# Optimization experiments

Hardware: AMD Instinct MI355X
Metric: run time of the kernel (lower is better)

The kernel has to match this reference:

```python
import jax, jax.numpy as jnp
import numpy as np

B, L, N = 16, 512, 32          # batch, seq_length, feature_size
E = 128                        # embed_size == frequency_size (number_frequency=1)
EMB = 8                        # embedding_dim
FCH = 64                       # fc_hidden_dim
H = 256                        # hidden_size
PRE = 96                       # pre_length
LAMBDA = 0.01                  # sparsity_threshold
SCALE = 0.02                   # init_scale


def softshrink(v, lambd=LAMBDA):
    return jnp.where(v > lambd, v - lambd, jnp.where(v < -lambd, v + lambd, 0.0))


def setup_inputs() -> dict:
    key = jax.random.key(0)
    ks = jax.random.split(key, 16)
    f32 = jnp.float32
    return {
        "x": jax.random.normal(ks[0], (B, L, N), f32),
        "emb": jax.random.normal(ks[1], (1, E), f32),
        "w0": SCALE * jax.random.normal(ks[2], (2, E, E), f32),
        "b0": SCALE * jax.random.normal(ks[3], (2, E), f32),
        "w1": SCALE * jax.random.normal(ks[4], (2, E, E), f32),
        "b1": SCALE * jax.random.normal(ks[5], (2, E), f32),
        "w2": SCALE * jax.random.normal(ks[6], (2, E, E), f32),
        "b2": SCALE * jax.random.normal(ks[7], (2, E), f32),
        "emb10": jax.random.normal(ks[8], (L, EMB), f32),
        "fc1_w": jax.random.normal(ks[9], (FCH, E * EMB), f32) / np.sqrt(E * EMB),
        "fc1_b": jnp.zeros((FCH,), f32),
        "fc2_w": jax.random.normal(ks[10], (H, FCH), f32) / np.sqrt(FCH),
        "fc2_b": jnp.zeros((H,), f32),
        "fc3_w": jax.random.normal(ks[11], (PRE, H), f32) / np.sqrt(H),
        "fc3_b": jnp.zeros((PRE,), f32),
    }


def _diag(w):
    # einsum 'bli,ii->bli' multiplies by the DIAGONAL of w only
    return jnp.diagonal(w, axis1=-2, axis2=-1)


def reference(x, emb, w0, b0, w1, b1, w2, b2, emb10,
              fc1_w, fc1_b, fc2_w, fc2_b, fc3_w, fc3_b):
    Bb = x.shape[0]
    xt = jnp.transpose(x, (0, 2, 1)).reshape(Bb, -1)          # [B, N*L]
    tok = xt[:, :, None] * emb                                 # [B, N*L, E]
    xf = jnp.fft.rfft(tok, axis=1, norm="ortho")               # [B, N*L//2+1, E] complex
    bias = xf

    # --- fourierGC (faithful to the torch op ordering, incl. o_real reuse) ---
    relu = jax.nn.relu
    d00, d01 = _diag(w0[0]), _diag(w0[1])
    o_r = relu(xf.real * d00 - xf.imag * d01 + b0[0])
    o_i = relu(xf.imag * d00 + xf.real * d01 + b0[1])
    prev = softshrink(jnp.stack([o_r, o_i], axis=-1))

    # middle layer (num_layers=3 -> one): note o_i uses the UPDATED o_r, as in torch
    d10, d11 = _diag(w1[0]), _diag(w1[1])
    o_r_new = relu(o_r * d10 - o_i * d11 + b1[0])
    o_i = relu(o_i * d10 + o_r_new * d11 + b1[1])
    o_r = o_r_new
    prev = softshrink(jnp.stack([o_r, o_i], axis=-1)) + prev

    # last layer
    d20, d21 = _diag(w2[0]), _diag(w2[1])
    o_r_new = relu(o_r * d20 - o_i * d21 + b2[0])
    o_i = relu(o_i * d20 + o_r_new * d21 + b2[1])
    z = softshrink(jnp.stack([o_r_new, o_i], axis=-1)) + prev
    zc = jax.lax.complex(z[..., 0], z[..., 1])

    xf = zc + bias
    xt = jnp.fft.irfft(xf, n=N * L, axis=1, norm="ortho")      # [B, N*L, E]
    xt = xt.reshape(Bb, N, L, E)
    xt = jnp.transpose(xt, (0, 1, 3, 2))                        # [B, N, E, L]
    h = jnp.matmul(xt, emb10)                                   # [B, N, E, EMB]
    h = h.reshape(Bb, N, E * EMB)

    lrelu = lambda v: jax.nn.leaky_relu(v, 0.01)
    h = lrelu(h @ fc1_w.T + fc1_b)
    h = lrelu(h @ fc2_w.T + fc2_b)
    out = h @ fc3_w.T + fc3_b                                   # [B, N, PRE]
    return out[:, 0, :]                                         # target_idx = 0
```

## Files before the change

### kernel.cpp

```cpp
#include <hip/hip_runtime.h>
#include <math.h>

#define Bsz   16
#define Lseq  512
#define Nfeat 32
#define E     128
#define EMB   8
#define FCH   64
#define Hd    256
#define PRE   96
#define M     16384
#define MH    8193
#define LAMBDA 0.01f

#define OFF_G   0
#define OFF_CS  524288
#define OFF_P   655376

#define TWO_PI_M   3.83495196971410293e-4f
#define TWO_PI_128 4.90873852123405245e-2f

__global__ __launch_bounds__(256)
void k_prep(const float* __restrict__ x, const float* __restrict__ emb10,
            float* __restrict__ ws) {
  __shared__ float smem[Lseq * EMB];
  int bid = blockIdx.x, tid = threadIdx.x;
  if (bid < 1025) {
    for (int i = tid; i < Lseq * EMB; i += 256) smem[i] = emb10[i];
    __syncthreads();
    int floc = tid >> 5, tl = tid & 31;
    int f = bid * 8 + floc;
    if (f > 8192) return;
    float ca[EMB], sa[EMB];
    #pragma unroll
    for (int m = 0; m < EMB; ++m) { ca[m] = 0.f; sa[m] = 0.f; }
    #pragma unroll 4
    for (int i = 0; i < 16; ++i) {
      int t = tl + 32 * i;
      int k = (f * t) & (M - 1);
      float ss, cc;
      sincosf((float)k * TWO_PI_M, &ss, &cc);
      const float* er = smem + t * EMB;
      #pragma unroll
      for (int m = 0; m < EMB; ++m) {
        ca[m] = fmaf(cc, er[m], ca[m]);
        sa[m] = fmaf(ss, er[m], sa[m]);
      }
    }
    #pragma unroll
    for (int off = 16; off >= 1; off >>= 1) {
      #pragma unroll
      for (int m = 0; m < EMB; ++m) {
        ca[m] += __shfl_xor(ca[m], off, 64);
        sa[m] += __shfl_xor(sa[m], off, 64);
      }
    }
    if (tl == 0) {
      float wf = (f == 0 || f == 8192) ? (1.0f / 128.0f) : (2.0f / 128.0f);
      float* o = ws + OFF_CS + f * 16;
      #pragma unroll
      for (int m = 0; m < EMB; ++m) { o[m] = ca[m] * wf; o[8 + m] = sa[m] * wf; }
    }
  } else {
    int v = bid - 1025;
    int b = v >> 6, t1base = (v & 63) << 1;
    int t1loc = tid >> 7, idx = tid & 127;
    {
      int t = (t1base + t1loc) + 128 * idx;
      int n = t >> 9, l = t & 511;
      smem[t1loc * 128 + idx] = x[b * (Lseq * Nfeat) + l * Nfeat + n];
    }
    __syncthreads();
    int f1 = idx, t1 = t1base + t1loc;
    float s1, c1; sincosf((float)f1 * TWO_PI_128, &s1, &c1);
    float c2 = c1 * c1 - s1 * s1, s2 = 2.f * s1 * c1;
    float cA = 1.f, sA = 0.f, cB = c1, sB = s1;
    float grA = 0.f, giA = 0.f, grB = 0.f, giB = 0.f;
    const float* xc = smem + t1loc * 128;
    #pragma unroll 8
    for (int t2 = 0; t2 < 128; t2 += 2) {
      float x0 = xc[t2], x1 = xc[t2 + 1];
      grA = fmaf(x0, cA, grA); giA = fmaf(x0, -sA, giA);
      grB = fmaf(x1, cB, grB); giB = fmaf(x1, -sB, giB);
      float cn = cA * c2 - sA * s2; sA = sA * c2 + cA * s2; cA = cn;
      cn = cB * c2 - sB * s2;       sB = sB * c2 + cB * s2; cB = cn;
    }
    float gr = grA + grB, gi = giA + giB;
    float sb, cb; sincosf((float)(f1 * t1) * TWO_PI_M, &sb, &cb);
    float grr = gr * cb + gi * sb;
    float gii = gi * cb - gr * sb;
    float* G = ws + OFF_G + ((b * 128 + f1) * 128 + t1) * 2;
    G[0] = grr;
    G[1] = gii;
  }
}

__global__ __launch_bounds__(256)
void k_gcf(const float* __restrict__ emb,
           const float* __restrict__ w0, const float* __restrict__ b0,
           const float* __restrict__ w1, const float* __restrict__ b1,
           const float* __restrict__ w2, const float* __restrict__ b2,
           float* __restrict__ ws) {
  int f1 = blockIdx.x, b = blockIdx.y, tid = threadIdx.x;
  int nf2 = (f1 == 0) ? 65 : 64;
  __shared__ float2 Gs[128];
  __shared__ float Xp[4][65][2];
  __shared__ float CSs[65 * 16];
  {
    const float2* gsrc = (const float2*)(ws + OFF_G + (b * 128 + f1) * 256);
    if (tid < 128) Gs[tid] = gsrc[tid];
    for (int j = tid; j < nf2 * 16; j += 256) {
      int i = j >> 4, m = j & 15;
      CSs[j] = ws[OFF_CS + (f1 + 128 * i) * 16 + m];
    }
  }
  __syncthreads();
  {
    int f2 = tid & 63, q = tid >> 6;
    int r = (f2 * q) & 3;
    float c = (r == 0) ? 1.f : (r == 2) ? -1.f : 0.f;
    float s = (r == 1) ? 1.f : (r == 3) ? -1.f : 0.f;
    float s1, c1; sincosf((float)f2 * TWO_PI_128, &s1, &c1);
    float xr = 0.f, xi = 0.f;
    int t1 = q * 32;
    #pragma unroll 8
    for (int k = 0; k < 32; ++k) {
      float2 g = Gs[t1 + k];
      xr = fmaf(g.x, c, xr); xr = fmaf(g.y, s, xr);
      xi = fmaf(g.y, c, xi); xi = fmaf(-g.x, s, xi);
      float cn = c * c1 - s * s1; s = s * c1 + c * s1; c = cn;
    }
    Xp[q][f2][0] = xr; Xp[q][f2][1] = xi;
    if (f1 == 0 && f2 == 0) {
      float er = 0.f, ei = 0.f;
      #pragma unroll 8
      for (int k = 0; k < 32; ++k) {
        float2 g = Gs[t1 + k];
        float sg = ((t1 + k) & 1) ? -1.f : 1.f;
        er = fmaf(g.x, sg, er); ei = fmaf(g.y, sg, ei);
      }
      Xp[q][64][0] = er; Xp[q][64][1] = ei;
    }
  }
  __syncthreads();
  int e = tid & 127, fh = tid >> 7;
  float se  = emb[e] * (1.0f / 128.0f);
  float d00 = w0[e * 129], d01 = w0[E * E + e * 129];
  float c00 = b0[e],       c01 = b0[E + e];
  float d10 = w1[e * 129], d11 = w1[E * E + e * 129];
  float c10 = b1[e],       c11 = b1[E + e];
  float d20 = w2[e * 129], d21 = w2[E * E + e * 129];
  float c20 = b2[e],       c21 = b2[E + e];
  float acc[EMB];
  #pragma unroll
  for (int m = 0; m < EMB; ++m) acc[m] = 0.f;

  for (int i = fh; i < nf2; i += 2) {
    float xr = ((Xp[0][i][0] + Xp[1][i][0]) + (Xp[2][i][0] + Xp[3][i][0])) * se;
    float xi = ((Xp[0][i][1] + Xp[1][i][1]) + (Xp[2][i][1] + Xp[3][i][1])) * se;
    float or0 = fmaxf(fmaf(xr, d00, fmaf(-xi, d01, c00)), 0.f);
    float oi0 = fmaxf(fmaf(xi, d00, fmaf(xr, d01, c01)), 0.f);
    float pr = fmaxf(or0 - LAMBDA, 0.f), pi = fmaxf(oi0 - LAMBDA, 0.f);
    float or1 = fmaxf(fmaf(or0, d10, fmaf(-oi0, d11, c10)), 0.f);
    float oi1 = fmaxf(fmaf(oi0, d10, fmaf(or1, d11, c11)), 0.f);
    pr += fmaxf(or1 - LAMBDA, 0.f); pi += fmaxf(oi1 - LAMBDA, 0.f);
    float or2 = fmaxf(fmaf(or1, d20, fmaf(-oi1, d21, c20)), 0.f);
    float oi2 = fmaxf(fmaf(oi1, d20, fmaf(or2, d21, c21)), 0.f);
    float zr = fmaxf(or2 - LAMBDA, 0.f) + pr;
    float zi = fmaxf(oi2 - LAMBDA, 0.f) + pi;
    const float* cs = &CSs[i * 16];
    #pragma unroll
    for (int m = 0; m < EMB; ++m)
      acc[m] = fmaf(zr, cs[m], fmaf(-zi, cs[8 + m], acc[m]));
  }
  __syncthreads();
  float* red = CSs;
  if (fh == 1) {
    #pragma unroll
    for (int m = 0; m < EMB; ++m) red[e * EMB + m] = acc[m];
  }
  __syncthreads();
  if (fh == 0) {
    float* P = ws + OFF_P + (f1 * 16 + b) * (E * EMB) + e * EMB;
    #pragma unroll
    for (int m = 0; m < EMB; ++m) P[m] = acc[m] + red[e * EMB + m];
  }
}

__global__ __launch_bounds__(256)
void k_fc(const float* __restrict__ x, const float* __restrict__ emb,
          const float* __restrict__ emb10,
          const float* __restrict__ fc1w, const float* __restrict__ fc1b,
          const float* __restrict__ fc2w, const float* __restrict__ fc2b,
          const float* __restrict__ fc3w, const float* __restrict__ fc3b,
          const float* __restrict__ ws, float* __restrict__ out) {
  int b = blockIdx.x;
  __shared__ float h0s[E * EMB];
  __shared__ float h1s[FCH];
  __shared__ float h2s[Hd];
  __shared__ float hxs[EMB];
  __shared__ float scratch[256];
  int tid = threadIdx.x;
  {
    int m = tid & 7, g = tid >> 3;
    float p = 0.f;
    for (int l = g; l < Lseq; l += 32)
      p = fmaf(x[b * (Lseq * Nfeat) + l * Nfeat], emb10[l * EMB + m], p);
    scratch[tid] = p;
  }
  __syncthreads();
  if (tid < 8) {
    float s = 0.f;
    for (int g = 0; g < 32; ++g) s += scratch[g * 8 + tid];
    hxs[tid] = s;
  }
  __syncthreads();
  for (int k = tid; k < E * EMB; k += 256) {
    float a = emb[k >> 3] * hxs[k & 7];
    const float* P = ws + OFF_P + b * (E * EMB) + k;
    #pragma unroll 16
    for (int c = 0; c < 128; ++c) a += P[c * (16 * E * EMB)];
    h0s[k] = a;
  }
  __syncthreads();
  {
    int o = tid & 63, kc = tid >> 6;
    const float* wrow = fc1w + o * (E * EMB) + kc * 256;
    const float* hh = h0s + kc * 256;
    float a = 0.f;
    #pragma unroll 8
    for (int k = 0; k < 256; ++k) a = fmaf(hh[k], wrow[k], a);
    scratch[tid] = a;
  }
  __syncthreads();
  if (tid < FCH) {
    float a = fc1b[tid] + scratch[tid] + scratch[tid + 64] +
              scratch[tid + 128] + scratch[tid + 192];
    h1s[tid] = a > 0.f ? a : 0.01f * a;
  }
  __syncthreads();
  {
    float a = fc2b[tid];
    const float* wrow = fc2w + tid * FCH;
    #pragma unroll 8
    for (int c = 0; c < FCH; ++c) a = fmaf(h1s[c], wrow[c], a);
    h2s[tid] = a > 0.f ? a : 0.01f * a;
  }
  __syncthreads();
  {
    int o = tid & 127, kc = tid >> 7;
    float a = 0.f;
    if (o < PRE) {
      const float* wrow = fc3w + o * Hd + kc * 128;
      const float* hh = h2s + kc * 128;
      #pragma unroll 8
      for (int k = 0; k < 128; ++k) a = fmaf(hh[k], wrow[k], a);
    }
    scratch[tid] = a;
  }
  __syncthreads();
  if (tid < PRE) out[b * PRE + tid] = fc3b[tid] + scratch[tid] + scratch[tid + 128];
}

extern "C" void kernel_launch(void* const* d_in, const int* in_sizes, int n_in,
                              void* d_out, int out_size, void* d_ws, size_t ws_size,
                              hipStream_t stream) {
  const float* x     = (const float*)d_in[0];
  const float* emb   = (const float*)d_in[1];
  const float* w0    = (const float*)d_in[2];
  const float* b0    = (const float*)d_in[3];
  const float* w1    = (const float*)d_in[4];
  const float* b1    = (const float*)d_in[5];
  const float* w2    = (const float*)d_in[6];
  const float* b2    = (const float*)d_in[7];
  const float* emb10 = (const float*)d_in[8];
  const float* fc1w  = (const float*)d_in[9];
  const float* fc1b  = (const float*)d_in[10];
  const float* fc2w  = (const float*)d_in[11];
  const float* fc2b  = (const float*)d_in[12];
  const float* fc3w  = (const float*)d_in[13];
  const float* fc3b  = (const float*)d_in[14];
  float* ws  = (float*)d_ws;
  float* out = (float*)d_out;

  k_prep<<<dim3(2049), 256, 0, stream>>>(x, emb10, ws);
  k_gcf<<<dim3(128, Bsz), 256, 0, stream>>>(emb, w0, b0, w1, b1, w2, b2, ws);
  k_fc<<<dim3(Bsz), 256, 0, stream>>>(x, emb, emb10, fc1w, fc1b, fc2w, fc2b,
                                      fc3w, fc3b, ws, out);
}
```

Before: 176.6 us.

## Split partial-sum reduction into its own kernel and widen FC stage

Moves the 128-way reduction of per-frequency partials out of the 16-block FC kernel into a new 256-block reduction kernel that writes h0 to workspace. The FC kernel now runs with 1024 threads and uses wave-level shuffle reductions for each output row, reading weights in a coalesced pattern. k_prep packs 4 frequencies per block to cut block count and redundant shared-memory loads of emb10. This exposes far more parallelism in the formerly serial tail, at the cost of an extra launch and a workspace round trip.

```diff
diff --git a/kernel.cpp b/kernel.cpp
--- a/kernel.cpp
+++ b/kernel.cpp
@@ -16,6 +16,7 @@
 #define OFF_G   0
 #define OFF_CS  524288
 #define OFF_P   655376
+#define OFF_H0  2752528
 
 #define TWO_PI_M   3.83495196971410293e-4f
 #define TWO_PI_128 4.90873852123405245e-2f
@@ -25,44 +26,48 @@
             float* __restrict__ ws) {
   __shared__ float smem[Lseq * EMB];
   int bid = blockIdx.x, tid = threadIdx.x;
-  if (bid < 1025) {
+  if (bid < 257) {
     for (int i = tid; i < Lseq * EMB; i += 256) smem[i] = emb10[i];
     __syncthreads();
     int floc = tid >> 5, tl = tid & 31;
-    int f = bid * 8 + floc;
-    if (f > 8192) return;
-    float ca[EMB], sa[EMB];
-    #pragma unroll
-    for (int m = 0; m < EMB; ++m) { ca[m] = 0.f; sa[m] = 0.f; }
-    #pragma unroll 4
-    for (int i = 0; i < 16; ++i) {
-      int t = tl + 32 * i;
-      int k = (f * t) & (M - 1);
-      float ss, cc;
-      sincosf((float)k * TWO_PI_M, &ss, &cc);
-      const float* er = smem + t * EMB;
-      #pragma unroll
-      for (int m = 0; m < EMB; ++m) {
-        ca[m] = fmaf(cc, er[m], ca[m]);
-        sa[m] = fmaf(ss, er[m], sa[m]);
+    #pragma unroll
+    for (int ff = 0; ff < 4; ++ff) {
+      int f = bid * 32 + ff * 8 + floc;
+      if (f <= 8192) {
+        float ca[EMB], sa[EMB];
+        #pragma unroll
+        for (int m = 0; m < EMB; ++m) { ca[m] = 0.f; sa[m] = 0.f; }
+        #pragma unroll 4
+        for (int i = 0; i < 16; ++i) {
+          int t = tl + 32 * i;
+          int k = (f * t) & (M - 1);
+          float ss, cc;
+          sincosf((float)k * TWO_PI_M, &ss, &cc);
+          const float* er = smem + t * EMB;
+          #pragma unroll
+          for (int m = 0; m < EMB; ++m) {
+            ca[m] = fmaf(cc, er[m], ca[m]);
+            sa[m] = fmaf(ss, er[m], sa[m]);
+          }
+        }
+        #pragma unroll
+        for (int off = 16; off >= 1; off >>= 1) {
+          #pragma unroll
+          for (int m = 0; m < EMB; ++m) {
+            ca[m] += __shfl_xor(ca[m], off, 64);
+            sa[m] += __shfl_xor(sa[m], off, 64);
+          }
+        }
+        if (tl == 0) {
+          float wf = (f == 0 || f == 8192) ? (1.0f / 128.0f) : (2.0f / 128.0f);
+          float* o = ws + OFF_CS + f * 16;
+          #pragma unroll
+          for (int m = 0; m < EMB; ++m) { o[m] = ca[m] * wf; o[8 + m] = sa[m] * wf; }
+        }
       }
     }
-    #pragma unroll
-    for (int off = 16; off >= 1; off >>= 1) {
-      #pragma unroll
-      for (int m = 0; m < EMB; ++m) {
-        ca[m] += __shfl_xor(ca[m], off, 64);
-        sa[m] += __shfl_xor(sa[m], off, 64);
-      }
-    }
-    if (tl == 0) {
-      float wf = (f == 0 || f == 8192) ? (1.0f / 128.0f) : (2.0f / 128.0f);
-      float* o = ws + OFF_CS + f * 16;
-      #pragma unroll
-      for (int m = 0; m < EMB; ++m) { o[m] = ca[m] * wf; o[8 + m] = sa[m] * wf; }
-    }
   } else {
-    int v = bid - 1025;
+    int v = bid - 257;
     int b = v >> 6, t1base = (v & 63) << 1;
     int t1loc = tid >> 7, idx = tid & 127;
     {
@@ -188,6 +193,25 @@
 }
 
 __global__ __launch_bounds__(256)
+void k_red(float* __restrict__ ws) {
+  int bid = blockIdx.x;
+  int b = bid >> 4, kq = bid & 15;
+  int tid = threadIdx.x;
+  int kk = tid & 63, f1g = tid >> 6;
+  int k = kq * 64 + kk;
+  const float* P = ws + OFF_P + b * (E * EMB) + k;
+  float a = 0.f;
+  #pragma unroll 8
+  for (int j = 0; j < 32; ++j)
+    a += P[(f1g * 32 + j) * (16 * E * EMB)];
+  __shared__ float sh[256];
+  sh[tid] = a;
+  __syncthreads();
+  if (tid < 64)
+    ws[OFF_H0 + b * (E * EMB) + k] = sh[tid] + sh[tid + 64] + sh[tid + 128] + sh[tid + 192];
+}
+
+__global__ __launch_bounds__(1024)
 void k_fc(const float* __restrict__ x, const float* __restrict__ emb,
           const float* __restrict__ emb10,
           const float* __restrict__ fc1w, const float* __restrict__ fc1b,
@@ -199,67 +223,59 @@
   __shared__ float h1s[FCH];
   __shared__ float h2s[Hd];
   __shared__ float hxs[EMB];
-  __shared__ float scratch[256];
+  __shared__ float scratch[1024];
   int tid = threadIdx.x;
+  int lane = tid & 63, w = tid >> 6;
   {
     int m = tid & 7, g = tid >> 3;
     float p = 0.f;
-    for (int l = g; l < Lseq; l += 32)
+    #pragma unroll
+    for (int l = g; l < Lseq; l += 128)
       p = fmaf(x[b * (Lseq * Nfeat) + l * Nfeat], emb10[l * EMB + m], p);
     scratch[tid] = p;
   }
   __syncthreads();
   if (tid < 8) {
     float s = 0.f;
-    for (int g = 0; g < 32; ++g) s += scratch[g * 8 + tid];
+    #pragma unroll 16
+    for (int g = 0; g < 128; ++g) s += scratch[g * 8 + tid];
     hxs[tid] = s;
   }
   __syncthreads();
-  for (int k = tid; k < E * EMB; k += 256) {
-    float a = emb[k >> 3] * hxs[k & 7];
-    const float* P = ws + OFF_P + b * (E * EMB) + k;
-    #pragma unroll 16
-    for (int c = 0; c < 128; ++c) a += P[c * (16 * E * EMB)];
-    h0s[k] = a;
-  }
-  __syncthreads();
-  {
-    int o = tid & 63, kc = tid >> 6;
-    const float* wrow = fc1w + o * (E * EMB) + kc * 256;
-    const float* hh = h0s + kc * 256;
+  h0s[tid] = ws[OFF_H0 + b * (E * EMB) + tid] + emb[tid >> 3] * hxs[tid & 7];
+  __syncthreads();
+  #pragma unroll
+  for (int oo = 0; oo < 4; ++oo) {
+    int o = oo * 16 + w;
+    const float* wr = fc1w + o * (E * EMB);
     float a = 0.f;
-    #pragma unroll 8
-    for (int k = 0; k < 256; ++k) a = fmaf(hh[k], wrow[k], a);
-    scratch[tid] = a;
-  }
-  __syncthreads();
-  if (tid < FCH) {
-    float a = fc1b[tid] + scratch[tid] + scratch[tid + 64] +
-              scratch[tid + 128] + scratch[tid + 192];
-    h1s[tid] = a > 0.f ? a : 0.01f * a;
-  }
-  __syncthreads();
-  {
-    float a = fc2b[tid];
-    const float* wrow = fc2w + tid * FCH;
-    #pragma unroll 8
-    for (int c = 0; c < FCH; ++c) a = fmaf(h1s[c], wrow[c], a);
-    h2s[tid] = a > 0.f ? a : 0.01f * a;
-  }
-  __syncthreads();
-  {
-    int o = tid & 127, kc = tid >> 7;
+    #pragma unroll
+    for (int j = 0; j < 16; ++j) a = fmaf(h0s[lane + 64 * j], wr[lane + 64 * j], a);
+    #pragma unroll
+    for (int off = 32; off >= 1; off >>= 1) a += __shfl_xor(a, off, 64);
+    if (lane == 0) { float v = a + fc1b[o]; h1s[o] = v > 0.f ? v : 0.01f * v; }
+  }
+  __syncthreads();
+  #pragma unroll
+  for (int oo = 0; oo < 16; ++oo) {
+    int o = oo * 16 + w;
+    float a = h1s[lane] * fc2w[o * FCH + lane];
+    #pragma unroll
+    for (int off = 32; off >= 1; off >>= 1) a += __shfl_xor(a, off, 64);
+    if (lane == 0) { float v = a + fc2b[o]; h2s[o] = v > 0.f ? v : 0.01f * v; }
+  }
+  __syncthreads();
+  #pragma unroll
+  for (int oo = 0; oo < 6; ++oo) {
+    int o = oo * 16 + w;
+    const float* wr = fc3w + o * Hd;
     float a = 0.f;
-    if (o < PRE) {
-      const float* wrow = fc3w + o * Hd + kc * 128;
-      const float* hh = h2s + kc * 128;
-      #pragma unroll 8
-      for (int k = 0; k < 128; ++k) a = fmaf(hh[k], wrow[k], a);
-    }
-    scratch[tid] = a;
-  }
-  __syncthreads();
-  if (tid < PRE) out[b * PRE + tid] = fc3b[tid] + scratch[tid] + scratch[tid + 128];
+    #pragma unroll
+    for (int j = 0; j < 4; ++j) a = fmaf(h2s[lane + 64 * j], wr[lane + 64 * j], a);
+    #pragma unroll
+    for (int off = 32; off >= 1; off >>= 1) a += __shfl_xor(a, off, 64);
+    if (lane == 0) out[b * PRE + o] = a + fc3b[o];
+  }
 }
 
 extern "C" void kernel_launch(void* const* d_in, const int* in_sizes, int n_in,
@@ -283,8 +299,9 @@
   float* ws  = (float*)d_ws;
   float* out = (float*)d_out;
 
-  k_prep<<<dim3(2049), 256, 0, stream>>>(x, emb10, ws);
+  k_prep<<<dim3(1281), 256, 0, stream>>>(x, emb10, ws);
   k_gcf<<<dim3(128, Bsz), 256, 0, stream>>>(emb, w0, b0, w1, b1, w2, b2, ws);
-  k_fc<<<dim3(Bsz), 256, 0, stream>>>(x, emb, emb10, fc1w, fc1b, fc2w, fc2b,
-                                      fc3w, fc3b, ws, out);
-}
+  k_red<<<dim3(256), 256, 0, stream>>>(ws);
+  k_fc<<<dim3(Bsz), 1024, 0, stream>>>(x, emb, emb10, fc1w, fc1b, fc2w, fc2b,
+                                       fc3w, fc3b, ws, out);
+}
```

Measured after the change: 160.5 us. 1.1x faster.
